# Optimization experiments

Hardware: AMD Instinct MI355X
Metric: run time of the kernel (lower is better)

## Reference

```python
import jax, jax.numpy as jnp
import numpy as np

FEA, DK, H = 512, 64, 8
B, L = 4, 2048
EPS = 1e-5


def _layernorm(x, g, b):
    mu = jnp.mean(x, axis=-1, keepdims=True)
    var = jnp.mean(jnp.square(x - mu), axis=-1, keepdims=True)
    return (x - mu) * jax.lax.rsqrt(var + EPS) * g + b


def setup_inputs() -> dict:
    key = jax.random.key(0)
    ks = jax.random.split(key, 12)
    d = {
        'qx': jax.random.normal(ks[0], (B, L, FEA), jnp.float32),
        'kx': jax.random.normal(ks[1], (B, L, FEA), jnp.float32),
        'vx': jax.random.normal(ks[2], (B, L, FEA), jnp.float32),
        'maskPAD': jax.random.randint(ks[3], (B, L, L), 0, 2, jnp.int32),
        # attention projections (stored as [in, out]); biases zero-init as in module
        'wq': jax.random.normal(ks[4], (FEA, DK * H), jnp.float32) * 0.02,
        'bq': jnp.zeros((DK * H,), jnp.float32),
        'wk': jax.random.normal(ks[5], (FEA, DK * H), jnp.float32) * 0.02,
        'bk': jnp.zeros((DK * H,), jnp.float32),
        'wv': jax.random.normal(ks[6], (FEA, DK * H), jnp.float32) * 0.02,
        'bv': jnp.zeros((DK * H,), jnp.float32),
        'wo': jax.random.normal(ks[7], (DK * H, FEA), jnp.float32) * 0.02,
        'bo': jnp.zeros((FEA,), jnp.float32),
        # FFN
        'w1': jax.random.normal(ks[8], (FEA, 4 * FEA), jnp.float32) * 0.02,
        'b1': jnp.zeros((4 * FEA,), jnp.float32),
        'w2': jax.random.normal(ks[9], (4 * FEA, FEA), jnp.float32) * 0.02,
        'b2': jnp.zeros((FEA,), jnp.float32),
        # layer norms
        'ln1_g': jnp.ones((FEA,), jnp.float32),
        'ln1_b': jnp.zeros((FEA,), jnp.float32),
        'ln2_g': jnp.ones((FEA,), jnp.float32),
        'ln2_b': jnp.zeros((FEA,), jnp.float32),
    }
    return d


def reference(qx, kx, vx, maskPAD, wq, bq, wk, bk, wv, bv, wo, bo,
              w1, b1, w2, b2, ln1_g, ln1_b, ln2_g, ln2_b):
    b, l, _ = qx.shape
    # project and split heads: [B, H, L, DK]
    q = (qx @ wq + bq).reshape(b, l, H, DK).transpose(0, 2, 1, 3)
    k = (kx @ wk + bk).reshape(b, l, H, DK).transpose(0, 2, 1, 3)
    v = (vx @ wv + bv).reshape(b, l, H, DK).transpose(0, 2, 1, 3)
    scores = jnp.einsum('bhqd,bhkd->bhqk', q, k) / np.sqrt(DK)  # [B,H,L,L]
    mask = (maskPAD == 0)[:, None, :, :]
    scores = jnp.where(mask, jnp.float32(-2 ** 15 + 1), scores)
    alpha = jax.nn.softmax(scores, axis=-1)
    z = jnp.einsum('bhqk,bhkd->bhqd', alpha, v)  # [B,H,L,DK]
    z = z.transpose(0, 2, 1, 3).reshape(b, l, H * DK)
    z = z @ wo + bo
    # post-LN FFN block (dropout = identity at inference)
    zn = _layernorm(vx + z, ln1_g, ln1_b)
    ffn = jax.nn.gelu(zn @ w1 + b1, approximate=False) @ w2 + b2
    return _layernorm(zn + ffn, ln2_g, ln2_b)
```

## Files before the change

kernel.cpp:

```cpp
#include <hip/hip_runtime.h>
#include <cstdint>


typedef __bf16 bf16;
typedef __bf16 bf16x8 __attribute__((ext_vector_type(8)));
typedef __bf16 bf16x2 __attribute__((ext_vector_type(2)));
typedef float floatx4 __attribute__((ext_vector_type(4)));
typedef unsigned uint2v __attribute__((ext_vector_type(2)));

__device__ __forceinline__ floatx4 mfma_bf16(bf16x8 a, bf16x8 b, floatx4 c) {
  return __builtin_amdgcn_mfma_f32_16x16x32_bf16(a, b, c, 0, 0, 0);
}

__device__ __forceinline__ void load_lds_16(const void* g, void* l) {
  auto gp = reinterpret_cast<const void __attribute__((address_space(1)))*>(
      reinterpret_cast<uintptr_t>(g));
  auto lp = reinterpret_cast<void __attribute__((address_space(3)))*>(
      (unsigned int)reinterpret_cast<uintptr_t>(l));
  __builtin_amdgcn_global_load_lds(gp, lp, 16, 0, 0);
}

__device__ __forceinline__ unsigned pack2(float a, float b) {
  bf16x2 p;
  p[0] = (bf16)a;
  p[1] = (bf16)b;
  return __builtin_bit_cast(unsigned, p);
}

__device__ __forceinline__ float gelu_f(float x) {
  float t = 0.7978845608f * (x + 0.044715f * x * x * x);
  float e = __builtin_amdgcn_exp2f(t * 2.885390082f);
  float th = 1.0f - 2.0f * __builtin_amdgcn_rcpf(e + 1.0f);
  return 0.5f * x * (1.0f + th);
}

#define PLANE128 2064
#define PLANE64 1040
#define KVCH 8320

__global__ void __launch_bounds__(256) prep_k(
    const float* __restrict__ wq, const float* __restrict__ wk,
    const float* __restrict__ wv, const float* __restrict__ wo,
    bf16* __restrict__ wqT, bf16* __restrict__ wkT, bf16* __restrict__ wvT,
    bf16* __restrict__ woT, const float* __restrict__ w1,
    bf16* __restrict__ w1T, const float* __restrict__ w2,
    bf16* __restrict__ w2T, const int* __restrict__ mpad,
    unsigned long long* __restrict__ mbits, const float* __restrict__ qx,
    const float* __restrict__ kx, const float* __restrict__ vx,
    bf16* __restrict__ xb) {
  __shared__ float tile[32][33];
  int bid = blockIdx.x, tid = threadIdx.x;
  int tx = tid & 31, ty = tid >> 5;
  if (bid < 3072) {
    const float* in;
    bf16* out;
    int m0, k0, K, M;
    if (bid < 1024) {
      int z = bid >> 8, r = bid & 255;
      in = (z == 0) ? wq : (z == 1) ? wk : (z == 2) ? wv : wo;
      out = (z == 0) ? wqT : (z == 1) ? wkT : (z == 2) ? wvT : woT;
      m0 = (r & 15) * 32; k0 = (r >> 4) * 32; K = 512; M = 512;
    } else if (bid < 2048) {
      int r = bid - 1024;
      in = w1; out = w1T;
      m0 = (r & 63) * 32; k0 = (r >> 6) * 32; K = 512; M = 2048;
    } else {
      int r = bid - 2048;
      in = w2; out = w2T;
      m0 = (r & 15) * 32; k0 = (r >> 4) * 32; K = 2048; M = 512;
    }
    for (int i = ty; i < 32; i += 8)
      tile[i][tx] = in[(size_t)(k0 + i) * M + m0 + tx];
    __syncthreads();
    for (int i = ty; i < 32; i += 8)
      out[(size_t)(m0 + i) * K + k0 + tx] = (bf16)tile[tx][i];
  } else if (bid < 5120) {
    int r = bid - 3072;
    int w0 = r * 128 + (tid >> 6) * 32;
    int lane = tid & 63;
#pragma unroll 4
    for (int i = 0; i < 32; ++i) {
      int w = w0 + i;
      int v = mpad[(size_t)w * 64 + lane];
      unsigned long long bmask = __ballot(v != 0);
      if (lane == 0) mbits[w] = bmask;
    }
  } else {
    int r = bid - 5120;
    size_t idx = ((size_t)r * 256 + tid) * 8;
    int sel = (int)(idx >> 22);
    size_t off = idx & ((1u << 22) - 1);
    const float* src = (sel == 0) ? qx : (sel == 1) ? kx : vx;
    float4 a = *(const float4*)(src + off);
    float4 b = *(const float4*)(src + off + 4);
    bf16x8 o;
    o[0] = (bf16)a.x; o[1] = (bf16)a.y; o[2] = (bf16)a.z; o[3] = (bf16)a.w;
    o[4] = (bf16)b.x; o[5] = (bf16)b.y; o[6] = (bf16)b.z; o[7] = (bf16)b.w;
    *(bf16x8*)(xb + idx) = o;
  }
}

template <int EPI>
__device__ __forceinline__ void epi_store(void* Cout, int n, int m, int M,
                                          float val) {
  if constexpr (EPI == 3) {
    ((bf16*)Cout)[(size_t)n * M + m] = (bf16)gelu_f(val);
  } else if constexpr (EPI == 4) {
    ((float*)Cout)[(size_t)n * M + m] = val;
  } else {
    ((float*)Cout)[(size_t)n * M + m] += val;
  }
}

template <int EPI, bool TALL>
__global__ void __launch_bounds__(256) gemm_bt(const bf16* __restrict__ A,
                                               const bf16* __restrict__ Bt,
                                               const float* __restrict__ bias,
                                               void* __restrict__ Cout,
                                               int M, int K, int lda, int ldb) {
  __shared__ __attribute__((aligned(16))) char As[2][4 * PLANE128];
  __shared__ __attribute__((aligned(16))) char Bs[2][TALL ? 4 * PLANE64
                                                         : 4 * PLANE128];
  int tid = threadIdx.x, wave = tid >> 6, lane = tid & 63;
  int lrow = lane & 15, quad = lane >> 4;
  int n0 = blockIdx.y * 128;
  int m0 = blockIdx.x * (TALL ? 64 : 128);
  int wr = wave >> 1, wc = wave & 1;
  floatx4 zero4 = {0.f, 0.f, 0.f, 0.f};
  constexpr int NI = TALL ? 2 : 4;
  floatx4 acc[NI][4];
#pragma unroll
  for (int i = 0; i < NI; ++i)
#pragma unroll
    for (int j = 0; j < 4; ++j) acc[i][j] = zero4;

  auto stage = [&](int buf, int k0) {
    int p = wave;
#pragma unroll
    for (int j = 0; j < 2; ++j) {
      int row = j * 64 + lane;
      load_lds_16(A + (size_t)(n0 + row) * lda + k0 + p * 8,
                  As[buf] + p * PLANE128 + j * 1024 + lane * 16);
    }
    if constexpr (TALL) {
      load_lds_16(Bt + (size_t)(m0 + lane) * ldb + k0 + p * 8,
                  Bs[buf] + p * PLANE64 + lane * 16);
    } else {
#pragma unroll
      for (int j = 0; j < 2; ++j) {
        int row = j * 64 + lane;
        load_lds_16(Bt + (size_t)(m0 + row) * ldb + k0 + p * 8,
                    Bs[buf] + p * PLANE128 + j * 1024 + lane * 16);
      }
    }
  };

  stage(0, 0);
  int nk = K >> 5;
  for (int t = 0; t < nk; ++t) {
    int cur = t & 1;
    __syncthreads();
    if (t + 1 < nk) stage(cur ^ 1, (t + 1) * 32);
    bf16x8 af[NI], bfr[4];
#pragma unroll
    for (int i = 0; i < NI; ++i) {
      int row = (TALL ? wave * 32 : wr * 64) + i * 16 + lrow;
      af[i] = *(const bf16x8*)(As[cur] + quad * PLANE128 + row * 16);
    }
#pragma unroll
    for (int j = 0; j < 4; ++j) {
      if constexpr (TALL)
        bfr[j] = *(const bf16x8*)(Bs[cur] + quad * PLANE64 +
                                  (j * 16 + lrow) * 16);
      else
        bfr[j] = *(const bf16x8*)(Bs[cur] + quad * PLANE128 +
                                  (wc * 64 + j * 16 + lrow) * 16);
    }
#pragma unroll
    for (int i = 0; i < NI; ++i)
#pragma unroll
      for (int j = 0; j < 4; ++j)
        acc[i][j] = mfma_bf16(af[i], bfr[j], acc[i][j]);
  }
  float bv[4];
#pragma unroll
  for (int j = 0; j < 4; ++j) {
    int m = m0 + (TALL ? 0 : wc * 64) + j * 16 + lrow;
    bv[j] = (EPI == 5) ? 0.f : bias[m];
  }
#pragma unroll
  for (int i = 0; i < NI; ++i)
#pragma unroll
    for (int j = 0; j < 4; ++j)
#pragma unroll
      for (int r = 0; r < 4; ++r) {
        int n = n0 + (TALL ? wave * 32 : wr * 64) + i * 16 + quad * 4 + r;
        int m = m0 + (TALL ? 0 : wc * 64) + j * 16 + lrow;
        epi_store<EPI>(Cout, n, m, M, acc[i][j][r] + bv[j]);
      }
}

__global__ void __launch_bounds__(256) qkv_k(const bf16* __restrict__ xb,
                                             const bf16* __restrict__ wqT,
                                             const bf16* __restrict__ wkT,
                                             const bf16* __restrict__ wvT,
                                             const float* __restrict__ bq,
                                             const float* __restrict__ bk,
                                             const float* __restrict__ bv_,
                                             bf16* __restrict__ qh,
                                             bf16* __restrict__ kh,
                                             bf16* __restrict__ vt) {
  __shared__ __attribute__((aligned(16))) char As[2][4 * PLANE128];
  __shared__ __attribute__((aligned(16))) char Bs[2][4 * PLANE128];
  int tid = threadIdx.x, wave = tid >> 6, lane = tid & 63;
  int lrow = lane & 15, quad = lane >> 4;
  int seg = blockIdx.y >> 6;
  int n0 = (blockIdx.y & 63) * 128, m0 = blockIdx.x * 128;
  const bf16* Af = xb + ((size_t)seg << 22);
  const bf16* Bt = (seg == 0) ? wqT : (seg == 1) ? wkT : wvT;
  const float* bias = (seg == 0) ? bq : (seg == 1) ? bk : bv_;
  bf16* out = (seg == 0) ? qh : (seg == 1) ? kh : vt;
  int wr = wave >> 1, wc = wave & 1;
  floatx4 zero4 = {0.f, 0.f, 0.f, 0.f};
  floatx4 acc[4][4];
#pragma unroll
  for (int i = 0; i < 4; ++i)
#pragma unroll
    for (int j = 0; j < 4; ++j) acc[i][j] = zero4;

  auto stage = [&](int buf, int k0) {
    int p = wave;
#pragma unroll
    for (int j = 0; j < 2; ++j) {
      int row = j * 64 + lane;
      load_lds_16(Af + (size_t)(n0 + row) * 512 + k0 + p * 8,
                  As[buf] + p * PLANE128 + j * 1024 + lane * 16);
      load_lds_16(Bt + (size_t)(m0 + row) * 512 + k0 + p * 8,
                  Bs[buf] + p * PLANE128 + j * 1024 + lane * 16);
    }
  };

  stage(0, 0);
  for (int t = 0; t < 16; ++t) {
    int cur = t & 1;
    __syncthreads();
    if (t < 15) stage(cur ^ 1, (t + 1) * 32);
    bf16x8 af[4], bfr[4];
#pragma unroll
    for (int i = 0; i < 4; ++i)
      af[i] = *(const bf16x8*)(As[cur] + quad * PLANE128 +
                               (wr * 64 + i * 16 + lrow) * 16);
#pragma unroll
    for (int j = 0; j < 4; ++j)
      bfr[j] = *(const bf16x8*)(Bs[cur] + quad * PLANE128 +
                                (wc * 64 + j * 16 + lrow) * 16);
#pragma unroll
    for (int i = 0; i < 4; ++i)
#pragma unroll
      for (int j = 0; j < 4; ++j) acc[i][j] = mfma_bf16(af[i], bfr[j], acc[i][j]);
  }
  float bvv[4];
#pragma unroll
  for (int j = 0; j < 4; ++j) bvv[j] = bias[m0 + wc * 64 + j * 16 + lrow];
  const float qscale = 0.1803368801f;
#pragma unroll
  for (int i = 0; i < 4; ++i)
#pragma unroll
    for (int j = 0; j < 4; ++j)
#pragma unroll
      for (int r = 0; r < 4; ++r) {
        int n = n0 + wr * 64 + i * 16 + quad * 4 + r;
        int m = m0 + wc * 64 + j * 16 + lrow;
        float val = acc[i][j][r] + bvv[j];
        int bb = n >> 11, l = n & 2047, hh = m >> 6, d = m & 63;
        if (seg == 0) {
          out[((size_t)((bb * 8 + hh) * 2048 + l)) * 64 + d] =
              (bf16)(val * qscale);
        } else {
          size_t tb_ = ((size_t)((bb * 8 + hh) * 32 + (l >> 6))) * 4096;
          if (seg == 1)
            out[tb_ + (d >> 3) * 512 + (l & 63) * 8 + (d & 7)] = (bf16)val;
          else
            out[tb_ + ((l >> 3) & 7) * 512 + d * 8 + (l & 7)] = (bf16)val;
        }
      }
}

__global__ void __launch_bounds__(512, 4) attn_k(const bf16* __restrict__ Qh,
                                                 const bf16* __restrict__ Kh,
                                                 const bf16* __restrict__ Vt,
                                                 const unsigned long long* __restrict__ MB,
                                                 bf16* __restrict__ Z) {
  __shared__ __attribute__((aligned(16))) char smem[8 * KVCH];
  int qt = blockIdx.x, h = blockIdx.y, b = blockIdx.z;
  int tid = threadIdx.x, wave = tid >> 6, lane = tid & 63;
  int hw = wave >> 2, wl = wave & 3;
  int lrow = lane & 15, quad = lane >> 4;
  int q0 = qt * 128;
  size_t headbase = (size_t)(b * 8 + h) * 2048 * 64;

  bf16x8 qf[2][2];
#pragma unroll
  for (int u = 0; u < 2; ++u) {
    const bf16* Qp =
        Qh + headbase + (size_t)(q0 + wl * 32 + u * 16 + lrow) * 64 + quad * 8;
    qf[u][0] = *(const bf16x8*)Qp;
    qf[u][1] = *(const bf16x8*)(Qp + 32);
  }

  floatx4 zero4 = {0.f, 0.f, 0.f, 0.f};
  floatx4 o_acc[2][4], acc_l[2];
#pragma unroll
  for (int u = 0; u < 2; ++u) {
    acc_l[u] = zero4;
#pragma unroll
    for (int dt = 0; dt < 4; ++dt) o_acc[u][dt] = zero4;
  }
  bf16x8 ones;
#pragma unroll
  for (int j = 0; j < 8; ++j) ones[j] = (bf16)1.0f;

  const bf16* Kt0 = Kh + headbase;
  const bf16* Vt0 = Vt + headbase;
  const uint2* MB0 =
      (const uint2*)(MB + ((size_t)b * 2048 + q0 + wl * 32 + lrow) * 32);
  int sh = quad * 4;

  char* KsH = smem + hw * 2 * KVCH;
  char* VsH = smem + 4 * KVCH + hw * 2 * KVCH;

  auto stage = [&](int buf, int kt) {
    const bf16* Ktile = Kt0 + (size_t)kt * 4096;
    const bf16* Vtile = Vt0 + (size_t)kt * 4096;
#pragma unroll
    for (int j = 0; j < 2; ++j) {
      int p = wl * 2 + j;
      load_lds_16(Ktile + p * 512 + lane * 8,
                  KsH + buf * KVCH + p * PLANE64 + lane * 16);
      load_lds_16(Vtile + p * 512 + lane * 8,
                  VsH + buf * KVCH + p * PLANE64 + lane * 16);
    }
  };

  int ktbase = hw * 16;
  stage(0, ktbase);
  uint2 mwc[2] = {MB0[ktbase], MB0[512 + ktbase]};

  for (int it = 0; it < 16; ++it) {
    int kt = ktbase + it;
    int cur = it & 1;
    __syncthreads();
    uint2 mwn[2];
    if (it < 15) {
      stage(cur ^ 1, kt + 1);
      mwn[0] = MB0[kt + 1];
      mwn[1] = MB0[512 + kt + 1];
    }
    const char* Kc = KsH + cur * KVCH;
    const char* Vc = VsH + cur * KVCH;
    unsigned S[2][4][2];
#pragma unroll
    for (int nt = 0; nt < 4; ++nt) {
      int R = nt * 16 + lrow;
      bf16x8 k0f = *(const bf16x8*)(Kc + quad * PLANE64 + R * 16);
      bf16x8 k1f = *(const bf16x8*)(Kc + (quad + 4) * PLANE64 + R * 16);
#pragma unroll
      for (int u = 0; u < 2; ++u) {
        floatx4 aa = zero4;
        aa = mfma_bf16(k0f, qf[u][0], aa);
        aa = mfma_bf16(k1f, qf[u][1], aa);
        unsigned wn = ((nt & 2) ? mwc[u].y : mwc[u].x) >> ((nt & 1) * 16 + sh);
        float e[4];
#pragma unroll
        for (int r = 0; r < 4; ++r)
          e[r] = (wn & (1u << r)) ? __builtin_amdgcn_exp2f(aa[r]) : 0.f;
        S[u][nt][0] = pack2(e[0], e[1]);
        S[u][nt][1] = pack2(e[2], e[3]);
      }
    }
    bf16x8 v0[4], v1[4];
#pragma unroll
    for (int dt = 0; dt < 4; ++dt) {
      int R = dt * 16 + lrow;
      v0[dt] = *(const bf16x8*)(Vc + quad * PLANE64 + R * 16);
      v1[dt] = *(const bf16x8*)(Vc + (quad + 4) * PLANE64 + R * 16);
    }
#pragma unroll
    for (int u = 0; u < 2; ++u) {
      union { unsigned w[4]; bf16x8 v; } pf[2];
#pragma unroll
      for (int half = 0; half < 2; ++half)
#pragma unroll
        for (int pr = 0; pr < 2; ++pr) {
          uint2v a = __builtin_amdgcn_permlane32_swap(
              S[u][half * 2][pr], S[u][half * 2 + 1][pr], false, false);
          uint2v c = __builtin_amdgcn_permlane16_swap(a[0], a[1], false, false);
          pf[half].w[pr] = c[0];
          pf[half].w[pr + 2] = c[1];
        }
      bf16x8 pf0 = pf[0].v, pf1 = pf[1].v;
      __builtin_amdgcn_s_setprio(1);
      acc_l[u] = mfma_bf16(pf0, ones, acc_l[u]);
      acc_l[u] = mfma_bf16(pf1, ones, acc_l[u]);
#pragma unroll
      for (int dt = 0; dt < 4; ++dt) {
        o_acc[u][dt] = mfma_bf16(pf0, v0[dt], o_acc[u][dt]);
        o_acc[u][dt] = mfma_bf16(pf1, v1[dt], o_acc[u][dt]);
      }
      __builtin_amdgcn_s_setprio(0);
    }
    if (it < 15) { mwc[0] = mwn[0]; mwc[1] = mwn[1]; }
  }

  __syncthreads();
  float* cb = (float*)smem;
  int cbase = (wl * 64 + lane) * 40;
  if (hw == 1) {
#pragma unroll
    for (int u = 0; u < 2; ++u) {
#pragma unroll
      for (int dt = 0; dt < 4; ++dt)
        *(floatx4*)(cb + cbase + (u * 4 + dt) * 4) = o_acc[u][dt];
      *(floatx4*)(cb + cbase + 32 + u * 4) = acc_l[u];
    }
  }
  __syncthreads();
  if (hw == 0) {
#pragma unroll
    for (int u = 0; u < 2; ++u) {
#pragma unroll
      for (int dt = 0; dt < 4; ++dt)
        o_acc[u][dt] += *(const floatx4*)(cb + cbase + (u * 4 + dt) * 4);
      acc_l[u] += *(const floatx4*)(cb + cbase + 32 + u * 4);
    }
#pragma unroll
    for (int u = 0; u < 2; ++u) {
      float lr[4];
#pragma unroll
      for (int r = 0; r < 4; ++r) lr[r] = 1.0f / acc_l[u][r];
#pragma unroll
      for (int dt = 0; dt < 4; ++dt)
#pragma unroll
        for (int r = 0; r < 4; ++r) {
          int qrow = q0 + wl * 32 + u * 16 + quad * 4 + r;
          int d = dt * 16 + lrow;
          Z[((size_t)(b * 2048 + qrow)) * 512 + h * 64 + d] =
              (bf16)(o_acc[u][dt][r] * lr[r]);
        }
    }
  }
}

template <bool A_BF16, bool OUT_BF16>
__global__ void __launch_bounds__(256) ln_k(const void* __restrict__ a_,
                                            const float* __restrict__ s,
                                            const float* __restrict__ g,
                                            const float* __restrict__ bta,
                                            void* __restrict__ out_) {
  int row = blockIdx.x * 4 + (threadIdx.x >> 6);
  int lane = threadIdx.x & 63;
  size_t base = (size_t)row * 512 + lane * 8;
  float x[8];
  float4 sa = *(const float4*)(s + base);
  float4 sb = *(const float4*)(s + base + 4);
  if constexpr (A_BF16) {
    bf16x8 av = *(const bf16x8*)((const bf16*)a_ + base);
    x[0] = (float)av[0] + sa.x; x[1] = (float)av[1] + sa.y;
    x[2] = (float)av[2] + sa.z; x[3] = (float)av[3] + sa.w;
    x[4] = (float)av[4] + sb.x; x[5] = (float)av[5] + sb.y;
    x[6] = (float)av[6] + sb.z; x[7] = (float)av[7] + sb.w;
  } else {
    float4 a0 = *(const float4*)((const float*)a_ + base);
    float4 a1 = *(const float4*)((const float*)a_ + base + 4);
    x[0] = a0.x + sa.x; x[1] = a0.y + sa.y; x[2] = a0.z + sa.z; x[3] = a0.w + sa.w;
    x[4] = a1.x + sb.x; x[5] = a1.y + sb.y; x[6] = a1.z + sb.z; x[7] = a1.w + sb.w;
  }
  float sum = 0.f;
#pragma unroll
  for (int i = 0; i < 8; ++i) sum += x[i];
#pragma unroll
  for (int off = 1; off < 64; off <<= 1) sum += __shfl_xor(sum, off, 64);
  float mu = sum * (1.0f / 512.0f);
  float vs = 0.f;
#pragma unroll
  for (int i = 0; i < 8; ++i) { float d = x[i] - mu; vs += d * d; }
#pragma unroll
  for (int off = 1; off < 64; off <<= 1) vs += __shfl_xor(vs, off, 64);
  float rstd = rsqrtf(vs * (1.0f / 512.0f) + 1e-5f);
  float4 g0 = *(const float4*)(g + lane * 8);
  float4 g1 = *(const float4*)(g + lane * 8 + 4);
  float4 b0 = *(const float4*)(bta + lane * 8);
  float4 b1 = *(const float4*)(bta + lane * 8 + 4);
  float gg[8] = {g0.x, g0.y, g0.z, g0.w, g1.x, g1.y, g1.z, g1.w};
  float bb[8] = {b0.x, b0.y, b0.z, b0.w, b1.x, b1.y, b1.z, b1.w};
  if constexpr (OUT_BF16) {
    bf16x8 o;
#pragma unroll
    for (int i = 0; i < 8; ++i)
      o[i] = (bf16)((x[i] - mu) * rstd * gg[i] + bb[i]);
    *(bf16x8*)((bf16*)out_ + base) = o;
  } else {
    float4 o0, o1;
    o0.x = (x[0] - mu) * rstd * gg[0] + bb[0];
    o0.y = (x[1] - mu) * rstd * gg[1] + bb[1];
    o0.z = (x[2] - mu) * rstd * gg[2] + bb[2];
    o0.w = (x[3] - mu) * rstd * gg[3] + bb[3];
    o1.x = (x[4] - mu) * rstd * gg[4] + bb[4];
    o1.y = (x[5] - mu) * rstd * gg[5] + bb[5];
    o1.z = (x[6] - mu) * rstd * gg[6] + bb[6];
    o1.w = (x[7] - mu) * rstd * gg[7] + bb[7];
    *(float4*)((float*)out_ + base) = o0;
    *(float4*)((float*)out_ + base + 4) = o1;
  }
}

extern "C" void kernel_launch(void* const* d_in, const int* in_sizes, int n_in,
                              void* d_out, int out_size, void* d_ws, size_t ws_size,
                              hipStream_t stream) {
  const float* qx = (const float*)d_in[0];
  const float* kx = (const float*)d_in[1];
  const float* vx = (const float*)d_in[2];
  const int* maskPAD = (const int*)d_in[3];
  const float* wq = (const float*)d_in[4];
  const float* bq = (const float*)d_in[5];
  const float* wk = (const float*)d_in[6];
  const float* bk = (const float*)d_in[7];
  const float* wv = (const float*)d_in[8];
  const float* bv = (const float*)d_in[9];
  const float* wo = (const float*)d_in[10];
  const float* bo = (const float*)d_in[11];
  const float* w1 = (const float*)d_in[12];
  const float* b1 = (const float*)d_in[13];
  const float* w2 = (const float*)d_in[14];
  const float* b2 = (const float*)d_in[15];
  const float* g1 = (const float*)d_in[16];
  const float* be1 = (const float*)d_in[17];
  const float* g2 = (const float*)d_in[18];
  const float* be2 = (const float*)d_in[19];

  char* w = (char*)d_ws;
  size_t off = 0;
  auto alloc = [&](size_t bytes) {
    void* p = w + off;
    off += (bytes + 255) & ~(size_t)255;
    return p;
  };
  bf16* wqT = (bf16*)alloc(512 * 512 * 2);
  bf16* wkT = (bf16*)alloc(512 * 512 * 2);
  bf16* wvT = (bf16*)alloc(512 * 512 * 2);
  bf16* woT = (bf16*)alloc(512 * 512 * 2);
  bf16* w1T = (bf16*)alloc(2048 * 512 * 2);
  bf16* w2T = (bf16*)alloc(512 * 2048 * 2);
  unsigned long long* mbits = (unsigned long long*)alloc((size_t)4 * 2048 * 32 * 8);
  bf16* xb = (bf16*)alloc((size_t)3 * 4194304 * 2);
  bf16* qh = (bf16*)alloc((size_t)8192 * 512 * 2);
  bf16* kh = (bf16*)alloc((size_t)8192 * 512 * 2);
  bf16* vt = (bf16*)alloc((size_t)8192 * 512 * 2);
  bf16* z = (bf16*)alloc((size_t)8192 * 512 * 2);
  float* s12 = (float*)qh;
  bf16* zn = vt;
  size_t h1_bytes = (size_t)8192 * 2048 * 2;
  bool big = (off + h1_bytes) <= ws_size;
  bf16* h1 = big ? (bf16*)alloc(h1_bytes) : z;

  prep_k<<<11264, 256, 0, stream>>>(wq, wk, wv, wo, wqT, wkT, wvT, woT, w1, w1T,
                                    w2, w2T, maskPAD, mbits, qx, kx, vx, xb);
  qkv_k<<<dim3(4, 192), 256, 0, stream>>>(xb, wqT, wkT, wvT, bq, bk, bv,
                                          qh, kh, vt);
  attn_k<<<dim3(16, 8, 4), 512, 0, stream>>>(qh, kh, vt, mbits, z);
  gemm_bt<4, true><<<dim3(8, 64), 256, 0, stream>>>(z, woT, bo, s12, 512, 512,
                                                    512, 512);
  ln_k<false, true><<<2048, 256, 0, stream>>>(vx, s12, g1, be1, zn);
  if (big) {
    gemm_bt<3, false><<<dim3(16, 64), 256, 0, stream>>>(zn, w1T, b1, h1, 2048,
                                                        512, 512, 512);
    gemm_bt<4, true><<<dim3(8, 64), 256, 0, stream>>>(h1, w2T, b2, s12, 512,
                                                      2048, 2048, 2048);
  } else {
    for (int p = 0; p < 4; ++p) {
      gemm_bt<3, true><<<dim3(8, 64), 256, 0, stream>>>(
          zn, w1T + (size_t)p * 512 * 512, b1 + p * 512, h1, 512, 512, 512, 512);
      if (p == 0)
        gemm_bt<4, true><<<dim3(8, 64), 256, 0, stream>>>(
            h1, w2T + p * 512, b2, s12, 512, 512, 512, 2048);
      else
        gemm_bt<5, true><<<dim3(8, 64), 256, 0, stream>>>(
            h1, w2T + p * 512, nullptr, s12, 512, 512, 512, 2048);
    }
  }
  ln_k<true, false><<<2048, 256, 0, stream>>>(zn, s12, g2, be2, (float*)d_out);
}
```

Baseline: 403.2 us.

## Store bf16 operands in 64x8 tiled layout for contiguous LDS staging

Introduces a tiled layout (64-row by 8-column blocks of 512 contiguous elements) for all bf16 GEMM operands: transposed weights, converted inputs, attention output, LN1 output and the GELU hidden activations. Each global_load_lds wave then reads one contiguous 1 KB chunk instead of 64 strided 16-byte pieces, which should improve coalescing and reduce address-translation overhead. Producers (prep, attention epilogue, LN, GELU epilogue) now write scattered 2-byte or 16-byte elements into the tiled layout. That may cost store efficiency, and the layout must stay consistent across every kernel. The K-split fallback path passes a kbase offset instead of a pointer offset.

```diff
diff --git a/kernel.cpp b/kernel.cpp
--- a/kernel.cpp
+++ b/kernel.cpp
@@ -18,6 +18,11 @@
   auto lp = reinterpret_cast<void __attribute__((address_space(3)))*>(
       (unsigned int)reinterpret_cast<uintptr_t>(l));
   __builtin_amdgcn_global_load_lds(gp, lp, 16, 0, 0);
+}
+
+__device__ __forceinline__ size_t tix(int row, int col, int C) {
+  return ((size_t)((row >> 6) * (C >> 3) + (col >> 3)) << 9) +
+         ((row & 63) << 3) + (col & 7);
 }
 
 __device__ __forceinline__ unsigned pack2(float a, float b) {
@@ -73,7 +78,7 @@
       tile[i][tx] = in[(size_t)(k0 + i) * M + m0 + tx];
     __syncthreads();
     for (int i = ty; i < 32; i += 8)
-      out[(size_t)(m0 + i) * K + k0 + tx] = (bf16)tile[tx][i];
+      out[tix(m0 + i, k0 + tx, K)] = (bf16)tile[tx][i];
   } else if (bid < 5120) {
     int r = bid - 3072;
     int w0 = r * 128 + (tid >> 6) * 32;
@@ -96,7 +101,8 @@
     bf16x8 o;
     o[0] = (bf16)a.x; o[1] = (bf16)a.y; o[2] = (bf16)a.z; o[3] = (bf16)a.w;
     o[4] = (bf16)b.x; o[5] = (bf16)b.y; o[6] = (bf16)b.z; o[7] = (bf16)b.w;
-    *(bf16x8*)(xb + idx) = o;
+    int row = (int)(off >> 9), k = (int)(off & 511);
+    *(bf16x8*)(xb + ((size_t)sel << 22) + tix(row, k, 512)) = o;
   }
 }
 
@@ -104,7 +110,7 @@
 __device__ __forceinline__ void epi_store(void* Cout, int n, int m, int M,
                                           float val) {
   if constexpr (EPI == 3) {
-    ((bf16*)Cout)[(size_t)n * M + m] = (bf16)gelu_f(val);
+    ((bf16*)Cout)[tix(n, m, M)] = (bf16)gelu_f(val);
   } else if constexpr (EPI == 4) {
     ((float*)Cout)[(size_t)n * M + m] = val;
   } else {
@@ -117,7 +123,8 @@
                                                const bf16* __restrict__ Bt,
                                                const float* __restrict__ bias,
                                                void* __restrict__ Cout,
-                                               int M, int K, int lda, int ldb) {
+                                               int M, int K, int lda, int ldb,
+                                               int kbase) {
   __shared__ __attribute__((aligned(16))) char As[2][4 * PLANE128];
   __shared__ __attribute__((aligned(16))) char Bs[2][TALL ? 4 * PLANE64
                                                          : 4 * PLANE128];
@@ -134,22 +141,23 @@
 #pragma unroll
     for (int j = 0; j < 4; ++j) acc[i][j] = zero4;
 
+  int ca = lda >> 3, cb = ldb >> 3;
   auto stage = [&](int buf, int k0) {
     int p = wave;
+    int kc = (k0 >> 3) + p;
+    int kcb = ((kbase + k0) >> 3) + p;
 #pragma unroll
     for (int j = 0; j < 2; ++j) {
-      int row = j * 64 + lane;
-      load_lds_16(A + (size_t)(n0 + row) * lda + k0 + p * 8,
+      load_lds_16(A + ((size_t)(((n0 >> 6) + j) * ca + kc) << 9) + lane * 8,
                   As[buf] + p * PLANE128 + j * 1024 + lane * 16);
     }
     if constexpr (TALL) {
-      load_lds_16(Bt + (size_t)(m0 + lane) * ldb + k0 + p * 8,
+      load_lds_16(Bt + ((size_t)((m0 >> 6) * cb + kcb) << 9) + lane * 8,
                   Bs[buf] + p * PLANE64 + lane * 16);
     } else {
 #pragma unroll
       for (int j = 0; j < 2; ++j) {
-        int row = j * 64 + lane;
-        load_lds_16(Bt + (size_t)(m0 + row) * ldb + k0 + p * 8,
+        load_lds_16(Bt + ((size_t)(((m0 >> 6) + j) * cb + kcb) << 9) + lane * 8,
                     Bs[buf] + p * PLANE128 + j * 1024 + lane * 16);
       }
     }
@@ -230,12 +238,12 @@
 
   auto stage = [&](int buf, int k0) {
     int p = wave;
+    int kc = (k0 >> 3) + p;
 #pragma unroll
     for (int j = 0; j < 2; ++j) {
-      int row = j * 64 + lane;
-      load_lds_16(Af + (size_t)(n0 + row) * 512 + k0 + p * 8,
+      load_lds_16(Af + ((size_t)(((n0 >> 6) + j) * 64 + kc) << 9) + lane * 8,
                   As[buf] + p * PLANE128 + j * 1024 + lane * 16);
-      load_lds_16(Bt + (size_t)(m0 + row) * 512 + k0 + p * 8,
+      load_lds_16(Bt + ((size_t)(((m0 >> 6) + j) * 64 + kc) << 9) + lane * 8,
                   Bs[buf] + p * PLANE128 + j * 1024 + lane * 16);
     }
   };
@@ -444,8 +452,8 @@
         for (int r = 0; r < 4; ++r) {
           int qrow = q0 + wl * 32 + u * 16 + quad * 4 + r;
           int d = dt * 16 + lrow;
-          Z[((size_t)(b * 2048 + qrow)) * 512 + h * 64 + d] =
-              (bf16)(o_acc[u][dt][r] * lr[r]);
+          int row = b * 2048 + qrow, col = h * 64 + d;
+          Z[tix(row, col, 512)] = (bf16)(o_acc[u][dt][r] * lr[r]);
         }
     }
   }
@@ -460,11 +468,12 @@
   int row = blockIdx.x * 4 + (threadIdx.x >> 6);
   int lane = threadIdx.x & 63;
   size_t base = (size_t)row * 512 + lane * 8;
+  size_t tbase = tix(row, lane * 8, 512);
   float x[8];
   float4 sa = *(const float4*)(s + base);
   float4 sb = *(const float4*)(s + base + 4);
   if constexpr (A_BF16) {
-    bf16x8 av = *(const bf16x8*)((const bf16*)a_ + base);
+    bf16x8 av = *(const bf16x8*)((const bf16*)a_ + tbase);
     x[0] = (float)av[0] + sa.x; x[1] = (float)av[1] + sa.y;
     x[2] = (float)av[2] + sa.z; x[3] = (float)av[3] + sa.w;
     x[4] = (float)av[4] + sb.x; x[5] = (float)av[5] + sb.y;
@@ -498,7 +507,7 @@
 #pragma unroll
     for (int i = 0; i < 8; ++i)
       o[i] = (bf16)((x[i] - mu) * rstd * gg[i] + bb[i]);
-    *(bf16x8*)((bf16*)out_ + base) = o;
+    *(bf16x8*)((bf16*)out_ + tbase) = o;
   } else {
     float4 o0, o1;
     o0.x = (x[0] - mu) * rstd * gg[0] + bb[0];
@@ -569,23 +578,24 @@
                                           qh, kh, vt);
   attn_k<<<dim3(16, 8, 4), 512, 0, stream>>>(qh, kh, vt, mbits, z);
   gemm_bt<4, true><<<dim3(8, 64), 256, 0, stream>>>(z, woT, bo, s12, 512, 512,
-                                                    512, 512);
+                                                    512, 512, 0);
   ln_k<false, true><<<2048, 256, 0, stream>>>(vx, s12, g1, be1, zn);
   if (big) {
     gemm_bt<3, false><<<dim3(16, 64), 256, 0, stream>>>(zn, w1T, b1, h1, 2048,
-                                                        512, 512, 512);
+                                                        512, 512, 512, 0);
     gemm_bt<4, true><<<dim3(8, 64), 256, 0, stream>>>(h1, w2T, b2, s12, 512,
-                                                      2048, 2048, 2048);
+                                                      2048, 2048, 2048, 0);
   } else {
     for (int p = 0; p < 4; ++p) {
       gemm_bt<3, true><<<dim3(8, 64), 256, 0, stream>>>(
-          zn, w1T + (size_t)p * 512 * 512, b1 + p * 512, h1, 512, 512, 512, 512);
+          zn, w1T + (size_t)p * 512 * 512, b1 + p * 512, h1, 512, 512, 512,
+          512, 0);
       if (p == 0)
         gemm_bt<4, true><<<dim3(8, 64), 256, 0, stream>>>(
-            h1, w2T + p * 512, b2, s12, 512, 512, 512, 2048);
+            h1, w2T, b2, s12, 512, 512, 512, 2048, p * 512);
       else
         gemm_bt<5, true><<<dim3(8, 64), 256, 0, stream>>>(
-            h1, w2T + p * 512, nullptr, s12, 512, 512, 512, 2048);
+            h1, w2T, nullptr, s12, 512, 512, 512, 2048, p * 512);
     }
   }
   ln_k<true, false><<<2048, 256, 0, stream>>>(zn, s12, g2, be2, (float*)d_out);
```

Result: faster. 381.8 us (-5.3%).
